# Kernel optimization log

Measured on AMD Instinct MI355X. Metric: run time of the kernel, lower is better.

## Reference

```python
import jax, jax.numpy as jnp
import numpy as np

B, T, C = 4, 2048, 1024
H = 16
D = C // H  # 64

def setup_inputs() -> dict:
    key = jax.random.key(0)
    k1, k2, k3, k4, k5 = jax.random.split(key, 5)
    s = 0.02
    return {
        "x": jax.random.normal(k1, (B, T, C), dtype=jnp.float32),
        "Wqkv": jax.random.normal(k2, (C, 3 * C), dtype=jnp.float32) * s,
        "bqkv": jnp.zeros((3 * C,), dtype=jnp.float32),
        "Wout": jax.random.normal(k3, (C, C), dtype=jnp.float32) * s,
        "bout": jnp.zeros((C,), dtype=jnp.float32),
    }

def reference(x, Wqkv, bqkv, Wout, bout):
    b, t, c = x.shape
    scale = D ** -0.5
    qkv = x @ Wqkv + bqkv                      # [B,T,3C]
    qkv = qkv.reshape(b, t, 3, H, D)
    q = qkv[:, :, 0].transpose(0, 2, 1, 3)     # [B,H,T,D]
    k = qkv[:, :, 1].transpose(0, 2, 1, 3)
    v = qkv[:, :, 2].transpose(0, 2, 1, 3)
    att = jnp.einsum('bhqd,bhkd->bhqk', q, k) * scale
    causal = jnp.tril(jnp.ones((t, t), dtype=bool))
    att = jnp.where(causal, att, -jnp.inf)
    att = jax.nn.softmax(att, axis=-1)
    y = jnp.einsum('bhqk,bhkd->bhqd', att, v)  # [B,H,T,D]
    y = y.transpose(0, 2, 1, 3).reshape(b, t, c)
    return y @ Wout + bout
```

## Files before the change

### kernel.cpp

```cpp
#include <hip/hip_runtime.h>
#include <hip/hip_bf16.h>


using f32x4 = __attribute__((ext_vector_type(4))) float;
using s16x8 = __attribute__((ext_vector_type(8))) short;
using s16x4 = __attribute__((ext_vector_type(4))) short;

#define MFMA16(a, b, c) __builtin_amdgcn_mfma_f32_16x16x32_bf16(a, b, c, 0, 0, 0)

__device__ __forceinline__ unsigned short f2bf(float f) {
    unsigned u = __builtin_bit_cast(unsigned, f);
    u += 0x7fffu + ((u >> 16) & 1u);
    return (unsigned short)(u >> 16);
}

__device__ __forceinline__ void gl_lds16(const void* g, void* l) {
    __builtin_amdgcn_global_load_lds(
        (const __attribute__((address_space(1))) void*)g,
        (__attribute__((address_space(3))) void*)l, 16, 0, 0);
}

__global__ __launch_bounds__(256) void cvt_x(const float* __restrict__ x,
                                             unsigned short* __restrict__ xb, int n4) {
    int i = blockIdx.x * 256 + threadIdx.x;
    if (i < n4) {
        f32x4 v = ((const f32x4*)x)[i];
        s16x4 o;
        o[0] = (short)f2bf(v[0]); o[1] = (short)f2bf(v[1]);
        o[2] = (short)f2bf(v[2]); o[3] = (short)f2bf(v[3]);
        ((s16x4*)xb)[i] = o;
    }
}

__global__ __launch_bounds__(256) void cvt_tr(const float* __restrict__ W,
                                              unsigned short* __restrict__ Wt,
                                              int R, int Cc) {
    __shared__ unsigned short tile[64][72];
    const int r0 = blockIdx.x * 64, c0 = blockIdx.y * 64;
    const int tid = threadIdx.x;
    const int r = tid >> 4, c4 = (tid & 15) * 4;
#pragma unroll
    for (int i = 0; i < 4; ++i) {
        f32x4 v = *(const f32x4*)(W + (size_t)(r0 + r + i * 16) * Cc + c0 + c4);
#pragma unroll
        for (int j = 0; j < 4; ++j) tile[r + i * 16][c4 + j] = f2bf(v[j]);
    }
    __syncthreads();
#pragma unroll
    for (int i = 0; i < 4; ++i) {
        s16x4 o;
#pragma unroll
        for (int j = 0; j < 4; ++j) o[j] = (short)tile[c4 + j][r + i * 16];
        *(s16x4*)(Wt + (size_t)(c0 + r + i * 16) * R + r0 + c4) = o;
    }
}

template <int MODE>
__global__ __launch_bounds__(256) void gemm_bt(
    const unsigned short* __restrict__ A, const unsigned short* __restrict__ Bt,
    const float* __restrict__ bias,
    unsigned short* __restrict__ qp, unsigned short* __restrict__ kp,
    unsigned short* __restrict__ vtp, float* __restrict__ outp,
    int M, int N, int K)
{
    __shared__ unsigned short As[128 * 32];
    __shared__ unsigned short Bs[128 * 32];
    const int tid  = threadIdx.x;
    const int lane = tid & 63, w = tid >> 6;
    const int wm = w >> 1, wn = w & 1;
    const int g = lane >> 4, li = lane & 15;
    const int m0 = blockIdx.x * 128, n0 = blockIdx.y * 128;
    const int srow = lane >> 2, sc = (lane & 3) * 8;

    f32x4 acc[4][4] = {};

    for (int k0 = 0; k0 < K; k0 += 32) {
        __syncthreads();
#pragma unroll
        for (int j = 0; j < 2; ++j) {
            const int rr = w * 32 + j * 16;
            gl_lds16(A  + (size_t)(m0 + rr + srow) * K + k0 + sc, As + rr * 32);
            gl_lds16(Bt + (size_t)(n0 + rr + srow) * K + k0 + sc, Bs + rr * 32);
        }
        __syncthreads();

        s16x8 af[4], bf[4];
#pragma unroll
        for (int i = 0; i < 4; ++i)
            af[i] = *(const s16x8*)(As + (wm * 64 + i * 16 + li) * 32 + g * 8);
#pragma unroll
        for (int i = 0; i < 4; ++i)
            bf[i] = *(const s16x8*)(Bs + (wn * 64 + i * 16 + li) * 32 + g * 8);
#pragma unroll
        for (int mi = 0; mi < 4; ++mi)
#pragma unroll
            for (int ni = 0; ni < 4; ++ni)
                acc[mi][ni] = MFMA16(af[mi], bf[ni], acc[mi][ni]);
    }

#pragma unroll
    for (int ni = 0; ni < 4; ++ni) {
        const int n = n0 + wn * 64 + ni * 16 + li;
        const float bv = bias[n];
        const int s = n >> 10, h = (n >> 6) & 15, d = n & 63;
#pragma unroll
        for (int mi = 0; mi < 4; ++mi) {
            const int mB = m0 + wm * 64 + mi * 16 + g * 4;
            float v0 = acc[mi][ni][0] + bv, v1 = acc[mi][ni][1] + bv;
            float v2 = acc[mi][ni][2] + bv, v3 = acc[mi][ni][3] + bv;
            if (MODE == 0) {
                const int b = mB >> 11, tt = mB & 2047;
                if (s == 2) {
                    unsigned pk01, pk23;
                    asm("v_cvt_pk_bf16_f32 %0, %1, %2" : "=v"(pk01) : "v"(v0), "v"(v1));
                    asm("v_cvt_pk_bf16_f32 %0, %1, %2" : "=v"(pk23) : "v"(v2), "v"(v3));
                    unsigned short* dst = vtp + ((size_t)(b * 16 + h) * 64 + d) * 2048 + tt;
                    *(unsigned*)dst = pk01;
                    *(unsigned*)(dst + 2) = pk23;
                } else {
                    const float sc2 = (s == 0) ? 0.1803368801111143f : 1.0f;
                    unsigned short* dst =
                        ((s == 0) ? qp : kp) + ((size_t)(b * 16 + h) * 2048 + tt) * 64 + d;
                    dst[0]   = f2bf(v0 * sc2);
                    dst[64]  = f2bf(v1 * sc2);
                    dst[128] = f2bf(v2 * sc2);
                    dst[192] = f2bf(v3 * sc2);
                }
            } else {
                float* dst = outp + (size_t)mB * N + n;
                dst[0] = v0; dst[N] = v1; dst[2 * N] = v2; dst[3 * N] = v3;
            }
        }
    }
}

__device__ __forceinline__ void stage_kv(
    const unsigned short* __restrict__ kb, const unsigned short* __restrict__ vtb,
    unsigned short* KsB, unsigned short* VsB, int kbase, int w, int lane)
{
    const int srow = lane >> 3;
    const int sw = ((lane & 7) ^ srow) * 8;
#pragma unroll
    for (int jj = 0; jj < 2; ++jj) {
        const int j = w * 2 + jj;
        const int row = j * 8 + srow;
        gl_lds16(kb  + (size_t)(kbase + row) * 64 + sw, KsB + j * 512);
        gl_lds16(vtb + (size_t)row * 2048 + kbase + sw, VsB + j * 512);
    }
}

__device__ __forceinline__ void qk_softmax(
    const unsigned short* Ks, const s16x8 qf0, const s16x8 qf1,
    f32x4 (&O)[4], float& m, float& l,
    unsigned short (*Psw)[72], s16x8& pf0, s16x8& pf1,
    int kbase, int wq0, int qrow, int g, int li)
{
    f32x4 sT[4];
    __builtin_amdgcn_s_setprio(1);
#pragma unroll
    for (int nf = 0; nf < 4; ++nf) {
        const int r = nf * 16 + li;
        s16x8 kf0 = *(const s16x8*)(Ks + r * 64 + ((g ^ (li & 7)) << 3));
        s16x8 kf1 = *(const s16x8*)(Ks + r * 64 + (((g + 4) ^ (li & 7)) << 3));
        f32x4 a = {};
        a = MFMA16(kf0, qf0, a);
        a = MFMA16(kf1, qf1, a);
        sT[nf] = a;
    }
    __builtin_amdgcn_s_setprio(0);

    if (kbase + 63 > wq0) {
#pragma unroll
        for (int nf = 0; nf < 4; ++nf)
#pragma unroll
            for (int r = 0; r < 4; ++r)
                if (kbase + nf * 16 + g * 4 + r > qrow) sT[nf][r] = -1e30f;
    }

    float t0 = fmaxf(fmaxf(sT[0][0], sT[0][1]), sT[0][2]);
    float t1 = fmaxf(fmaxf(sT[0][3], sT[1][0]), sT[1][1]);
    float t2 = fmaxf(fmaxf(sT[1][2], sT[1][3]), sT[2][0]);
    float t3 = fmaxf(fmaxf(sT[2][1], sT[2][2]), sT[2][3]);
    float t4 = fmaxf(fmaxf(sT[3][0], sT[3][1]), sT[3][2]);
    float mx = fmaxf(fmaxf(t0, t1), t2);
    mx = fmaxf(fmaxf(mx, t3), fmaxf(t4, sT[3][3]));
    mx = fmaxf(mx, __shfl_xor(mx, 16));
    mx = fmaxf(mx, __shfl_xor(mx, 32));

    if (__any(mx > m + 8.f)) {
        const float mnew = fmaxf(m, mx);
        const float fac  = __builtin_amdgcn_exp2f(m - mnew);
        m = mnew;
        l *= fac;
        float facr[4];
#pragma unroll
        for (int r = 0; r < 4; ++r) facr[r] = __shfl(fac, g * 4 + r);
#pragma unroll
        for (int nf = 0; nf < 4; ++nf)
#pragma unroll
            for (int r = 0; r < 4; ++r) O[nf][r] *= facr[r];
    }

    float rs = 0.f;
#pragma unroll
    for (int nf = 0; nf < 4; ++nf)
#pragma unroll
        for (int r = 0; r < 4; ++r) {
            float p = __builtin_amdgcn_exp2f(sT[nf][r] - m);
            sT[nf][r] = p;
            rs += p;
        }
    rs += __shfl_xor(rs, 16);
    rs += __shfl_xor(rs, 32);
    l += rs;

#pragma unroll
    for (int nf = 0; nf < 4; ++nf) {
        unsigned pk0, pk1;
        asm("v_cvt_pk_bf16_f32 %0, %1, %2" : "=v"(pk0) : "v"(sT[nf][0]), "v"(sT[nf][1]));
        asm("v_cvt_pk_bf16_f32 %0, %1, %2" : "=v"(pk1) : "v"(sT[nf][2]), "v"(sT[nf][3]));
        uint2 pv; pv.x = pk0; pv.y = pk1;
        *(uint2*)(&Psw[li][nf * 16 + g * 4]) = pv;
    }
    pf0 = *(const s16x8*)(&Psw[li][g * 8]);
    pf1 = *(const s16x8*)(&Psw[li][32 + g * 8]);
}

__global__ __launch_bounds__(256, 4) void attn_k(
    const unsigned short* __restrict__ qbuf,
    const unsigned short* __restrict__ kbuf,
    const unsigned short* __restrict__ vtbuf,
    unsigned short* __restrict__ ybuf)
{
    __shared__ unsigned short Ks[4096];
    __shared__ unsigned short Vs[4096];
    __shared__ unsigned short PsA[4][16][72];
    __shared__ unsigned short PsB[4][16][72];

    const int tid  = threadIdx.x;
    const int lane = tid & 63, w = tid >> 6;
    const int g = lane >> 4, li = lane & 15;

    const int id   = blockIdx.x;
    const int slot = id >> 3;
    const int bh   = (id & 7) * 8 + (slot & 7);
    const int bx   = slot >> 3;
    const int qtA  = 31 - bx, qtB = bx;

    const unsigned short* qb  = qbuf  + (size_t)bh * 131072;
    const unsigned short* kb  = kbuf  + (size_t)bh * 131072;
    const unsigned short* vtb = vtbuf + (size_t)bh * 131072;
    const int b = bh >> 4, h = bh & 15;

    const int wqA = qtA * 64 + w * 16, qrowA = wqA + li;
    const int wqB = qtB * 64 + w * 16, qrowB = wqB + li;

    const unsigned short* qrA = qb + (size_t)qrowA * 64 + g * 8;
    const s16x8 qfA0 = *(const s16x8*)qrA;
    const s16x8 qfA1 = *(const s16x8*)(qrA + 32);
    const unsigned short* qrB = qb + (size_t)qrowB * 64 + g * 8;
    const s16x8 qfB0 = *(const s16x8*)qrB;
    const s16x8 qfB1 = *(const s16x8*)(qrB + 32);

    f32x4 OA[4] = {}, OB[4] = {};
    float mA = -1e30f, lA = 0.f, mB = -1e30f, lB = 0.f;

    const int nkb = qtA + 1;
    stage_kv(kb, vtb, Ks, Vs, 0, w, lane);
    asm volatile("s_waitcnt vmcnt(0)" ::: "memory");
    __syncthreads();

    for (int t = 0; t < nkb; ++t) {
        const int kbase = t * 64;
        const bool actB = (t <= qtB);

        s16x8 pfA0, pfA1, pfB0, pfB1;
        qk_softmax(Ks, qfA0, qfA1, OA, mA, lA, &PsA[w][0], pfA0, pfA1,
                   kbase, wqA, qrowA, g, li);
        if (actB)
            qk_softmax(Ks, qfB0, qfB1, OB, mB, lB, &PsB[w][0], pfB0, pfB1,
                       kbase, wqB, qrowB, g, li);

        __builtin_amdgcn_s_setprio(1);
#pragma unroll
        for (int nf = 0; nf < 4; ++nf) {
            const int d = nf * 16 + li;
            s16x8 vf0 = *(const s16x8*)(Vs + d * 64 + ((g ^ (li & 7)) << 3));
            s16x8 vf1 = *(const s16x8*)(Vs + d * 64 + (((g + 4) ^ (li & 7)) << 3));
            OA[nf] = MFMA16(pfA0, vf0, OA[nf]);
            OA[nf] = MFMA16(pfA1, vf1, OA[nf]);
            if (actB) {
                OB[nf] = MFMA16(pfB0, vf0, OB[nf]);
                OB[nf] = MFMA16(pfB1, vf1, OB[nf]);
            }
        }
        __builtin_amdgcn_s_setprio(0);

        if (t + 1 < nkb) {
            __syncthreads();
            stage_kv(kb, vtb, Ks, Vs, kbase + 64, w, lane);
            asm volatile("s_waitcnt vmcnt(0)" ::: "memory");
            __syncthreads();
        }
    }

    {
        const float linv = __builtin_amdgcn_rcpf(lA);
        float lr[4];
#pragma unroll
        for (int r = 0; r < 4; ++r) lr[r] = __shfl(linv, g * 4 + r);
#pragma unroll
        for (int nf = 0; nf < 4; ++nf)
#pragma unroll
            for (int r = 0; r < 4; ++r) {
                const int row = wqA + g * 4 + r;
                ybuf[((size_t)(b * 2048 + row)) * 1024 + h * 64 + nf * 16 + li] =
                    f2bf(OA[nf][r] * lr[r]);
            }
    }
    {
        const float linv = __builtin_amdgcn_rcpf(lB);
        float lr[4];
#pragma unroll
        for (int r = 0; r < 4; ++r) lr[r] = __shfl(linv, g * 4 + r);
#pragma unroll
        for (int nf = 0; nf < 4; ++nf)
#pragma unroll
            for (int r = 0; r < 4; ++r) {
                const int row = wqB + g * 4 + r;
                ybuf[((size_t)(b * 2048 + row)) * 1024 + h * 64 + nf * 16 + li] =
                    f2bf(OB[nf][r] * lr[r]);
            }
    }
}

extern "C" void kernel_launch(void* const* d_in, const int* in_sizes, int n_in,
                              void* d_out, int out_size, void* d_ws, size_t ws_size,
                              hipStream_t stream)
{
    const float* x    = (const float*)d_in[0];
    const float* Wqkv = (const float*)d_in[1];
    const float* bqkv = (const float*)d_in[2];
    const float* Wout = (const float*)d_in[3];
    const float* bout = (const float*)d_in[4];

    unsigned short* ws0 = (unsigned short*)d_ws;
    unsigned short* ws1 = ws0 + (size_t)8388608;
    unsigned short* ws2 = ws0 + (size_t)2 * 8388608;
    unsigned short* ws3 = ws0 + (size_t)3 * 8388608;

    unsigned short* xbf   = (unsigned short*)d_out;
    unsigned short* WqkvT = xbf + (size_t)8388608;

    cvt_x<<<8192, 256, 0, stream>>>(x, xbf, 2097152);
    cvt_tr<<<dim3(16, 48), 256, 0, stream>>>(Wqkv, WqkvT, 1024, 3072);
    gemm_bt<0><<<dim3(64, 24), 256, 0, stream>>>(
        xbf, WqkvT, bqkv, ws0, ws1, ws2, nullptr, 8192, 3072, 1024);
    attn_k<<<1024, 256, 0, stream>>>(ws0, ws1, ws2, ws3);
    cvt_tr<<<dim3(16, 16), 256, 0, stream>>>(Wout, ws0, 1024, 1024);
    gemm_bt<1><<<dim3(64, 8), 256, 0, stream>>>(
        ws3, ws0, bout, nullptr, nullptr, nullptr, (float*)d_out, 8192, 1024, 1024);
}
```

Baseline: 178.1 us.

## Double-buffer GEMM LDS tiles with BK=64, XOR swizzle, and MFMA priority

The bf16 GEMM kernel used for the QKV and output projections now keeps two LDS stages of 128x64 tiles, so global-to-LDS loads for the next K tile overlap the MFMAs on the current one. The load address uses an XOR swizzle of the 16-byte chunk index by row to avoid LDS bank conflicts on fragment reads. MFMA sections are wrapped in s_setprio. LDS use grows to 64 KB per block, and the launch bound asks for 2 blocks per CU, which adds register-pressure risk.

```diff
diff --git a/kernel.cpp b/kernel.cpp
--- a/kernel.cpp
+++ b/kernel.cpp
@@ -56,46 +56,72 @@
 }
 
 template <int MODE>
-__global__ __launch_bounds__(256) void gemm_bt(
+__global__ __launch_bounds__(256, 2) void gemm_bt(
     const unsigned short* __restrict__ A, const unsigned short* __restrict__ Bt,
     const float* __restrict__ bias,
     unsigned short* __restrict__ qp, unsigned short* __restrict__ kp,
     unsigned short* __restrict__ vtp, float* __restrict__ outp,
     int M, int N, int K)
 {
-    __shared__ unsigned short As[128 * 32];
-    __shared__ unsigned short Bs[128 * 32];
+    __shared__ unsigned short As[2][128 * 64];
+    __shared__ unsigned short Bs[2][128 * 64];
+
     const int tid  = threadIdx.x;
     const int lane = tid & 63, w = tid >> 6;
     const int wm = w >> 1, wn = w & 1;
     const int g = lane >> 4, li = lane & 15;
     const int m0 = blockIdx.x * 128, n0 = blockIdx.y * 128;
-    const int srow = lane >> 2, sc = (lane & 3) * 8;
+
+    const int srow = lane >> 3;
+    const int ssw  = ((lane & 7) ^ srow) * 8;
 
     f32x4 acc[4][4] = {};
 
-    for (int k0 = 0; k0 < K; k0 += 32) {
+    auto STAGE = [&](int buf, int k0) {
+#pragma unroll
+        for (int j = 0; j < 4; ++j) {
+            const int rr = w * 32 + j * 8;
+            gl_lds16(A  + (size_t)(m0 + rr + srow) * K + k0 + ssw, &As[buf][rr * 64]);
+            gl_lds16(Bt + (size_t)(n0 + rr + srow) * K + k0 + ssw, &Bs[buf][rr * 64]);
+        }
+    };
+
+    STAGE(0, 0);
+    asm volatile("s_waitcnt vmcnt(0)" ::: "memory");
+    __syncthreads();
+
+    const int nt = K >> 6;
+    int cur = 0;
+    for (int t = 0; t < nt; ++t) {
+        if (t + 1 < nt) STAGE(cur ^ 1, (t + 1) << 6);
+
+        s16x8 af[4][2], bf[4][2];
+#pragma unroll
+        for (int i = 0; i < 4; ++i) {
+            const int ra = wm * 64 + i * 16 + li;
+            const int rb = wn * 64 + i * 16 + li;
+#pragma unroll
+            for (int kk = 0; kk < 2; ++kk) {
+                af[i][kk] = *(const s16x8*)(
+                    &As[cur][ra * 64 + (((kk * 4 + g) ^ (ra & 7)) << 3)]);
+                bf[i][kk] = *(const s16x8*)(
+                    &Bs[cur][rb * 64 + (((kk * 4 + g) ^ (rb & 7)) << 3)]);
+            }
+        }
+
+        __builtin_amdgcn_s_setprio(1);
+#pragma unroll
+        for (int kk = 0; kk < 2; ++kk)
+#pragma unroll
+            for (int mi = 0; mi < 4; ++mi)
+#pragma unroll
+                for (int ni = 0; ni < 4; ++ni)
+                    acc[mi][ni] = MFMA16(af[mi][kk], bf[ni][kk], acc[mi][ni]);
+        __builtin_amdgcn_s_setprio(0);
+
+        asm volatile("s_waitcnt vmcnt(0)" ::: "memory");
         __syncthreads();
-#pragma unroll
-        for (int j = 0; j < 2; ++j) {
-            const int rr = w * 32 + j * 16;
-            gl_lds16(A  + (size_t)(m0 + rr + srow) * K + k0 + sc, As + rr * 32);
-            gl_lds16(Bt + (size_t)(n0 + rr + srow) * K + k0 + sc, Bs + rr * 32);
-        }
-        __syncthreads();
-
-        s16x8 af[4], bf[4];
-#pragma unroll
-        for (int i = 0; i < 4; ++i)
-            af[i] = *(const s16x8*)(As + (wm * 64 + i * 16 + li) * 32 + g * 8);
-#pragma unroll
-        for (int i = 0; i < 4; ++i)
-            bf[i] = *(const s16x8*)(Bs + (wn * 64 + i * 16 + li) * 32 + g * 8);
-#pragma unroll
-        for (int mi = 0; mi < 4; ++mi)
-#pragma unroll
-            for (int ni = 0; ni < 4; ++ni)
-                acc[mi][ni] = MFMA16(af[mi], bf[ni], acc[mi][ni]);
+        cur ^= 1;
     }
 
 #pragma unroll
```

Result: faster. 167.9 us (-5.7%).
